# Kernel tuning notes

Measured on AMD Instinct MI355X. Metric: run time of the kernel, lower is better.

The kernel has to match this reference:

```python
import jax, jax.numpy as jnp
import numpy as np

N_SEG = 128      # number of ragged segments (boundaries has N_SEG+1 entries)
SEG_LEN = 128    # tokens per segment (regular boundaries)
D_IN = 1024      # input_size
H = 512          # hidden per direction; output_size = 2*H = 1024


def _run_dir(xs, W_ih, W_hh, b):
    """xs: [L, B, D] -> hidden states [L, B, H] for one direction.
    torch LSTM gate order: i, f, g, o."""
    xp = jnp.einsum('lbd,gd->lbg', xs, W_ih) + b  # precompute input projections [L,B,4H]
    B = xs.shape[1]
    Hh = W_hh.shape[1]

    def step(carry, gx):
        h, c = carry
        g = gx + h @ W_hh.T
        i, f, gg, o = jnp.split(g, 4, axis=-1)
        c = jax.nn.sigmoid(f) * c + jax.nn.sigmoid(i) * jnp.tanh(gg)
        h = jax.nn.sigmoid(o) * jnp.tanh(c)
        return (h, c), h

    z = jnp.zeros((B, Hh), xs.dtype)
    _, hs = jax.lax.scan(step, (z, z), xp)
    return hs


def _bilstm(x, W_ih_f, W_hh_f, b_f, W_ih_b, W_hh_b, b_b):
    hf = _run_dir(x, W_ih_f, W_hh_f, b_f)
    hb = _run_dir(x[::-1], W_ih_b, W_hh_b, b_b)[::-1]
    return jnp.concatenate([hf, hb], axis=-1)  # [L, B, 2H], fwd then bwd as in torch


def setup_inputs() -> dict:
    key = jax.random.key(0)
    ks = jax.random.split(key, 7)
    T = N_SEG * SEG_LEN
    s = 1.0 / np.sqrt(H)  # torch LSTM init scale
    u = lambda k, shape: jax.random.uniform(k, shape, jnp.float32, -s, s)
    return {
        'all_embs': jax.random.normal(ks[0], (T, D_IN), jnp.float32),
        'boundaries': jnp.arange(N_SEG + 1, dtype=jnp.int32) * SEG_LEN,
        'W_ih_f': u(ks[1], (4 * H, D_IN)),
        'W_hh_f': u(ks[2], (4 * H, H)),
        'b_f': u(ks[3], (4 * H,)),  # b_ih + b_hh folded together
        'W_ih_b': u(ks[4], (4 * H, D_IN)),
        'W_hh_b': u(ks[5], (4 * H, H)),
        'b_b': u(ks[6], (4 * H,)),
    }


def reference(all_embs, boundaries, W_ih_f, W_hh_f, b_f, W_ih_b, W_hh_b, b_b):
    n_seg = boundaries.shape[0] - 1
    T, D = all_embs.shape
    L = T // n_seg
    # regular boundaries: batch the per-segment LSTM calls into one scan
    x = all_embs.reshape(n_seg, L, D).transpose(1, 0, 2)  # [L, n_seg, D]
    y = _bilstm(x, W_ih_f, W_hh_f, b_f, W_ih_b, W_hh_b, b_b)  # [L, n_seg, 2H]
    out = y.transpose(1, 0, 2).reshape(T, 2 * H)
    # summarize=False: new boundaries equal old boundaries
    return (out, boundaries)
```

## Files before the change

kernel.cpp:

```cpp
#include <hip/hip_runtime.h>


typedef __attribute__((ext_vector_type(8))) short bf16x8;
typedef __attribute__((ext_vector_type(4))) float f32x4;

__device__ __forceinline__ unsigned short f2bf(float f) {
  unsigned int x = __builtin_bit_cast(unsigned int, f);
  x += 0x7fffu + ((x >> 16) & 1u);
  return (unsigned short)(x >> 16);
}
__device__ __forceinline__ float bf2f(unsigned short u) {
  unsigned int x = ((unsigned int)u) << 16;
  return __builtin_bit_cast(float, x);
}
__device__ __forceinline__ float sigm(float x) { return 1.f / (1.f + __expf(-x)); }
__device__ __forceinline__ float tanhfast(float x) {
  float e = __expf(2.f * x);
  return 1.f - 2.f / (e + 1.f);
}

__device__ __forceinline__ void gl_lds16(const void* g, void* l) {
  __builtin_amdgcn_global_load_lds((const __attribute__((address_space(1))) unsigned int*)g,
                                   (__attribute__((address_space(3))) unsigned int*)l, 16, 0, 0);
}
__device__ __forceinline__ void gl_lds16_llc(const void* g, void* l) {
  __builtin_amdgcn_global_load_lds((const __attribute__((address_space(1))) unsigned int*)g,
                                   (__attribute__((address_space(3))) unsigned int*)l, 16, 0, 17);
}

__global__ __launch_bounds__(256) void cast_x(const float* __restrict__ X,
                                              unsigned short* __restrict__ Xb) {
  const int i = blockIdx.x * 256 + threadIdx.x;
  const float4 v = ((const float4*)X)[i];
  uint2 o;
  o.x = (unsigned int)f2bf(v.x) | ((unsigned int)f2bf(v.y) << 16);
  o.y = (unsigned int)f2bf(v.z) | ((unsigned int)f2bf(v.w) << 16);
  ((uint2*)Xb)[i] = o;
}

__global__ __launch_bounds__(256) void pack_w(const float* __restrict__ Wif,
                                              const float* __restrict__ bf_,
                                              const float* __restrict__ Wib,
                                              const float* __restrict__ bb_,
                                              unsigned short* __restrict__ Wc,
                                              float* __restrict__ biasp) {
  const int pr = blockIdx.x;
  const int d = pr >> 11, r = pr & 2047;
  const float* src = (d ? Wib : Wif) + (size_t)r * 1024;
  const int t = threadIdx.x;
  const float4 v = ((const float4*)src)[t];
  uint2 o;
  o.x = (unsigned int)f2bf(v.x) | ((unsigned int)f2bf(v.y) << 16);
  o.y = (unsigned int)f2bf(v.z) | ((unsigned int)f2bf(v.w) << 16);
  ((uint2*)(Wc + (size_t)pr * 1024))[t] = o;
  if (t == 0) biasp[pr] = (d ? bb_ : bf_)[r];
}

__global__ __launch_bounds__(256) void gemm_xp(const unsigned short* __restrict__ A,
                                               const unsigned short* __restrict__ B,
                                               const float* __restrict__ bias,
                                               unsigned short* __restrict__ C) {
  __shared__ unsigned short As[128 * 64];
  __shared__ unsigned short Bs[128 * 64];
  const int tid = threadIdx.x;
  const int lane = tid & 63;
  const int wid = tid >> 6;
  const int wm = wid >> 1, wn = wid & 1;
  const long brow = (long)blockIdx.x * 128;
  const long bcol = (long)blockIdx.y * 128;

  f32x4 acc[4][4];
  const f32x4 z = {0.f, 0.f, 0.f, 0.f};
#pragma unroll
  for (int i = 0; i < 4; ++i)
#pragma unroll
    for (int j = 0; j < 4; ++j) acc[i][j] = z;

  int srow[4], scol[4];
#pragma unroll
  for (int j = 0; j < 4; ++j) {
    const int o = (j * 256 + tid) * 16;
    srow[j] = o >> 7;
    scol[j] = (o & 127) ^ ((srow[j] & 7) << 4);
  }

  for (int ks = 0; ks < 16; ++ks) {
    const int kb0 = ks * 128;
#pragma unroll
    for (int j = 0; j < 4; ++j) {
      const int o = (j * 256 + tid) * 16;
      gl_lds16((const char*)A + (brow + srow[j]) * 2048 + kb0 + scol[j], (char*)As + o);
      gl_lds16((const char*)B + (bcol + srow[j]) * 2048 + kb0 + scol[j], (char*)Bs + o);
    }
    __syncthreads();
    bf16x8 av[4][2], bv[4][2];
#pragma unroll
    for (int f = 0; f < 4; ++f) {
      const int ra = wm * 64 + f * 16 + (lane & 15);
      const int rb = wn * 64 + f * 16 + (lane & 15);
      const int swa = (ra & 7) << 4, swb = (rb & 7) << 4;
#pragma unroll
      for (int kk = 0; kk < 2; ++kk) {
        const int kby = kk * 64 + (lane >> 4) * 16;
        av[f][kk] = *(const bf16x8*)((const char*)As + ra * 128 + (kby ^ swa));
        bv[f][kk] = *(const bf16x8*)((const char*)Bs + rb * 128 + (kby ^ swb));
      }
    }
#pragma unroll
    for (int kk = 0; kk < 2; ++kk)
#pragma unroll
      for (int fm = 0; fm < 4; ++fm)
#pragma unroll
        for (int fn = 0; fn < 4; ++fn)
          acc[fm][fn] =
              __builtin_amdgcn_mfma_f32_16x16x32_bf16(av[fm][kk], bv[fn][kk], acc[fm][fn], 0, 0, 0);
    __syncthreads();
  }
  const int crow0 = wm * 64 + (lane >> 4) * 4;
  const int ccol0 = wn * 64 + (lane & 15);
#pragma unroll
  for (int fm = 0; fm < 4; ++fm) {
#pragma unroll
    for (int fn = 0; fn < 4; ++fn) {
      const long col = bcol + ccol0 + fn * 16;
      const float bsv = bias[col];
#pragma unroll
      for (int r = 0; r < 4; ++r) {
        const long row = brow + crow0 + fm * 16 + r;
        C[row * 4096 + col] = f2bf(acc[fm][fn][r] + bsv);
      }
    }
  }
}

__global__ __launch_bounds__(256, 1) void lstm_persist(
    const unsigned short* __restrict__ XPb, const float* __restrict__ Whf,
    const float* __restrict__ Whb, unsigned short* __restrict__ hb0,
    unsigned short* __restrict__ hb1, float* __restrict__ out,
    unsigned int* __restrict__ ctr) {
  __shared__ unsigned short A_s[8192];
  __shared__ unsigned short Hrep[16][32];

  const int tid = threadIdx.x;
  const int bid = blockIdx.x;
  const int ut = bid >> 4;
  const int grp = bid & 15;
  const int dir = grp >> 3;
  const int cs = grp & 7;
  const int lane = tid & 63;
  const int w = tid >> 6;
  const int p = lane & 15;
  const int kq8 = lane >> 4;
  const int hi = p >> 3;
  const int u_l = w * 8 + (p & 7);
  const int u_g = ut * 32 + u_l;
  unsigned int* const myctr = ctr + grp * 32;

  bf16x8 wreg[2][16];
  {
    const float* Wh = dir ? Whb : Whf;
#pragma unroll
    for (int f = 0; f < 2; ++f) {
      const int g = f * 2 + hi;
      const float* wrow = Wh + (size_t)(g * 512 + u_g) * 512 + kq8 * 8;
#pragma unroll
      for (int kk = 0; kk < 16; ++kk) {
        const float4 v0 = *(const float4*)(wrow + kk * 32);
        const float4 v1 = *(const float4*)(wrow + kk * 32 + 4);
        bf16x8 t;
        t[0] = (short)f2bf(v0.x); t[1] = (short)f2bf(v0.y);
        t[2] = (short)f2bf(v0.z); t[3] = (short)f2bf(v0.w);
        t[4] = (short)f2bf(v1.x); t[5] = (short)f2bf(v1.y);
        t[6] = (short)f2bf(v1.z); t[7] = (short)f2bf(v1.w);
        wreg[f][kk] = t;
      }
    }
  }

  float c_reg[2] = {0.f, 0.f};
  const size_t tileoff = (size_t)grp * 16384;
  const int cl0 = kq8 * 4 + 2 * hi;

  for (int tau = 0; tau < 128; ++tau) {
    const unsigned short* hc = (tau & 1) ? hb1 : hb0;
    unsigned short* hn = (tau & 1) ? hb0 : hb1;
    const int tcol = dir ? (127 - tau) : tau;

    {
      const char* srcb = (const char*)hc + tileoff;
      char* dstb = (char*)A_s;
#pragma unroll
      for (int j = 0; j < 4; ++j) {
        const int o = (j * 256 + tid) * 16;
        gl_lds16_llc(srcb + o, dstb + o);
      }
    }

    unsigned short xpr[2][4];
#pragma unroll
    for (int j = 0; j < 2; ++j) {
      const int seg = cs * 16 + cl0 + j;
      const size_t tok = (size_t)seg * 128 + tcol;
      const unsigned short* xp = XPb + tok * 4096 + dir * 2048 + u_g;
#pragma unroll
      for (int g = 0; g < 4; ++g) xpr[j][g] = xp[g * 512];
    }
    __syncthreads();

    f32x4 accp[2][2];
    const f32x4 z = {0.f, 0.f, 0.f, 0.f};
    accp[0][0] = z; accp[0][1] = z; accp[1][0] = z; accp[1][1] = z;
    {
      const char* abase = (const char*)A_s + p * 1024;
      const int asw = (p & 7) << 4;
#pragma unroll
      for (int kk = 0; kk < 16; ++kk) {
        const int kb = kk * 64 + kq8 * 16;
        const bf16x8 af = *(const bf16x8*)(abase + (kb ^ asw));
        accp[0][kk & 1] =
            __builtin_amdgcn_mfma_f32_16x16x32_bf16(af, wreg[0][kk], accp[0][kk & 1], 0, 0, 0);
        accp[1][kk & 1] =
            __builtin_amdgcn_mfma_f32_16x16x32_bf16(af, wreg[1][kk], accp[1][kk & 1], 0, 0, 0);
      }
    }
    f32x4 acc0, acc1;
#pragma unroll
    for (int r = 0; r < 4; ++r) {
      acc0[r] = accp[0][0][r] + accp[0][1][r];
      acc1[r] = accp[1][0][r] + accp[1][1][r];
    }

    float hvr[2];
    {
      const float s0 = hi ? acc0[0] : acc0[2];
      const float s1 = hi ? acc0[1] : acc0[3];
      const float s2 = hi ? acc1[0] : acc1[2];
      const float s3 = hi ? acc1[1] : acc1[3];
      const float e0 = __shfl_xor(s0, 8);
      const float e1 = __shfl_xor(s1, 8);
      const float e2 = __shfl_xor(s2, 8);
      const float e3 = __shfl_xor(s3, 8);
      const float a0 = hi ? acc0[2] : acc0[0];
      const float a1 = hi ? acc0[3] : acc0[1];
      const float b0 = hi ? acc1[2] : acc1[0];
      const float b1 = hi ? acc1[3] : acc1[1];
      const float gi[2] = {hi ? e0 : a0, hi ? e1 : a1};
      const float gf[2] = {hi ? a0 : e0, hi ? a1 : e1};
      const float gg[2] = {hi ? e2 : b0, hi ? e3 : b1};
      const float go[2] = {hi ? b0 : e2, hi ? b1 : e3};
#pragma unroll
      for (int j = 0; j < 2; ++j) {
        const int cl = cl0 + j;
        const float pi = gi[j] + bf2f(xpr[j][0]);
        const float pf = gf[j] + bf2f(xpr[j][1]);
        const float pg = gg[j] + bf2f(xpr[j][2]);
        const float po = go[j] + bf2f(xpr[j][3]);
        float cv = sigm(pf) * c_reg[j] + sigm(pi) * tanhfast(pg);
        c_reg[j] = cv;
        hvr[j] = sigm(po) * tanhfast(cv);
        Hrep[cl][u_l] = f2bf(hvr[j]);
      }
    }
    __syncthreads();

    if (tid < 128) {
      const int cl = tid >> 3, q = tid & 7;
      const unsigned long long v = *(const unsigned long long*)&Hrep[cl][q * 4];
      char* dst = (char*)hn + tileoff + cl * 1024 + ((ut * 64 + q * 8) ^ ((cl & 7) << 4));
      __hip_atomic_store((unsigned long long*)dst, v, __ATOMIC_RELAXED,
                         __HIP_MEMORY_SCOPE_AGENT);
    }

    __syncthreads();
    if (tid == 0) {
      const unsigned old =
          __hip_atomic_fetch_add(myctr, 1u, __ATOMIC_RELAXED, __HIP_MEMORY_SCOPE_AGENT);
      const unsigned tgt = (unsigned)(tau + 1) * 16u;
      if (old + 1u != tgt) {
        while (__hip_atomic_load(myctr, __ATOMIC_RELAXED, __HIP_MEMORY_SCOPE_AGENT) < tgt)
          __builtin_amdgcn_s_sleep(1);
      }
    }
#pragma unroll
    for (int j = 0; j < 2; ++j) {
      const int seg = cs * 16 + cl0 + j;
      const size_t tok = (size_t)seg * 128 + tcol;
      out[tok * 1024 + dir * 512 + u_g] = hvr[j];
    }
    __syncthreads();
  }
}

__global__ void wr_bounds(const int* __restrict__ b, float* __restrict__ o) {
  const int i = threadIdx.x;
  if (i < 129) o[i] = (float)b[i];
}

extern "C" void kernel_launch(void* const* d_in, const int* in_sizes, int n_in,
                              void* d_out, int out_size, void* d_ws, size_t ws_size,
                              hipStream_t stream) {
  const float* X = (const float*)d_in[0];
  const int* bnd = (const int*)d_in[1];
  const float* Wif = (const float*)d_in[2];
  const float* Whf = (const float*)d_in[3];
  const float* bf_ = (const float*)d_in[4];
  const float* Wib = (const float*)d_in[5];
  const float* Whb = (const float*)d_in[6];
  const float* bb_ = (const float*)d_in[7];
  float* out = (float*)d_out;

  wr_bounds<<<1, 256, 0, stream>>>(bnd, out + 16777216);

  char* ws = (char*)d_ws;
  const size_t NEED = 176703488ULL;
  if (ws_size < NEED) return;

  unsigned short* XPb = (unsigned short*)(ws + 0);
  unsigned short* Xb = (unsigned short*)(ws + 134217728);
  unsigned short* Wc = (unsigned short*)(ws + 167772160);
  float* biasp = (float*)(ws + 176160768);
  unsigned short* hb0 = (unsigned short*)(ws + 176177152);
  unsigned short* hb1 = (unsigned short*)(ws + 176439296);
  unsigned int* ctrp = (unsigned int*)(ws + 176701440);

  cast_x<<<16384, 256, 0, stream>>>(X, Xb);
  pack_w<<<4096, 256, 0, stream>>>(Wif, bf_, Wib, bb_, Wc, biasp);
  dim3 gg(128, 32);
  gemm_xp<<<gg, 256, 0, stream>>>(Xb, Wc, biasp, XPb);

  hipMemsetAsync(hb0, 0, 262144, stream);
  hipMemsetAsync(ctrp, 0, 2048, stream);

  {
    const unsigned short* xpb = XPb;
    const float* whf = Whf;
    const float* whb = Whb;
    unsigned short* h0 = hb0;
    unsigned short* h1 = hb1;
    float* op = out;
    unsigned int* cp = ctrp;
    void* args[] = {&xpb, &whf, &whb, &h0, &h1, &op, &cp};
    hipError_t e = hipLaunchCooperativeKernel((const void*)lstm_persist, dim3(256), dim3(256),
                                              args, 0, stream);
    if (e != hipSuccess) {
      lstm_persist<<<256, 256, 0, stream>>>(XPb, Whf, Whb, hb0, hb1, out, ctrp);
    }
  }
}
```

Before: 504.9 us.

## Prefetch next-step input projections, defer output stores, stage GEMM epilogue through LDS

The recurrent kernel now loads the next timestep's input-projection values one iteration ahead, so their global-load latency overlaps the current step's MFMA and gate math instead of sitting on the serial path. The output store of h for a step is deferred into the next iteration, after the LDS-load issue, which moves it off the critical path between the barrier spin and the next step. The projection GEMM epilogue writes bf16 results into shared memory and then emits coalesced 16-byte row stores instead of scattered 2-byte stores. In exchange, register pressure rises in the persistent kernel from the extra prefetch and deferred-store registers.

```diff
diff --git a/kernel.cpp b/kernel.cpp
--- a/kernel.cpp
+++ b/kernel.cpp
@@ -60,8 +60,9 @@
                                                const unsigned short* __restrict__ B,
                                                const float* __restrict__ bias,
                                                unsigned short* __restrict__ C) {
-  __shared__ unsigned short As[128 * 64];
-  __shared__ unsigned short Bs[128 * 64];
+  __shared__ unsigned short SMEM[16384];
+  unsigned short* As = SMEM;
+  unsigned short* Bs = SMEM + 8192;
   const int tid = threadIdx.x;
   const int lane = tid & 63;
   const int wid = tid >> 6;
@@ -122,14 +123,20 @@
   for (int fm = 0; fm < 4; ++fm) {
 #pragma unroll
     for (int fn = 0; fn < 4; ++fn) {
-      const long col = bcol + ccol0 + fn * 16;
-      const float bsv = bias[col];
-#pragma unroll
-      for (int r = 0; r < 4; ++r) {
-        const long row = brow + crow0 + fm * 16 + r;
-        C[row * 4096 + col] = f2bf(acc[fm][fn][r] + bsv);
-      }
-    }
+      const int col = ccol0 + fn * 16;
+      const float bsv = bias[bcol + col];
+#pragma unroll
+      for (int r = 0; r < 4; ++r)
+        SMEM[(crow0 + fm * 16 + r) * 128 + col] = f2bf(acc[fm][fn][r] + bsv);
+    }
+  }
+  __syncthreads();
+#pragma unroll
+  for (int j = 0; j < 8; ++j) {
+    const int id = j * 256 + tid;
+    const int row = id >> 4;
+    const int c = id & 15;
+    *(float4*)(C + (brow + row) * 4096 + bcol + c * 8) = *(const float4*)(SMEM + row * 128 + c * 8);
   }
 }
 
@@ -181,6 +188,22 @@
   const size_t tileoff = (size_t)grp * 16384;
   const int cl0 = kq8 * 4 + 2 * hi;
 
+  unsigned short xpr[2][4];
+  {
+    const int tcol0 = dir ? 127 : 0;
+#pragma unroll
+    for (int j = 0; j < 2; ++j) {
+      const int seg = cs * 16 + cl0 + j;
+      const size_t tok = (size_t)seg * 128 + tcol0;
+      const unsigned short* xp = XPb + tok * 4096 + dir * 2048 + u_g;
+#pragma unroll
+      for (int g = 0; g < 4; ++g) xpr[j][g] = xp[g * 512];
+    }
+  }
+
+  float phv[2];
+  size_t pofs[2] = {0, 0};
+
   for (int tau = 0; tau < 128; ++tau) {
     const unsigned short* hc = (tau & 1) ? hb1 : hb0;
     unsigned short* hn = (tau & 1) ? hb0 : hb1;
@@ -195,17 +218,24 @@
         gl_lds16_llc(srcb + o, dstb + o);
       }
     }
-
-    unsigned short xpr[2][4];
-#pragma unroll
-    for (int j = 0; j < 2; ++j) {
-      const int seg = cs * 16 + cl0 + j;
-      const size_t tok = (size_t)seg * 128 + tcol;
-      const unsigned short* xp = XPb + tok * 4096 + dir * 2048 + u_g;
-#pragma unroll
-      for (int g = 0; g < 4; ++g) xpr[j][g] = xp[g * 512];
-    }
-    __syncthreads();
+    if (tau > 0) {
+      out[pofs[0]] = phv[0];
+      out[pofs[1]] = phv[1];
+    }
+    __syncthreads();
+
+    unsigned short xprN[2][4];
+    if (tau < 127) {
+      const int tcolN = dir ? (126 - tau) : (tau + 1);
+#pragma unroll
+      for (int j = 0; j < 2; ++j) {
+        const int seg = cs * 16 + cl0 + j;
+        const size_t tok = (size_t)seg * 128 + tcolN;
+        const unsigned short* xp = XPb + tok * 4096 + dir * 2048 + u_g;
+#pragma unroll
+        for (int g = 0; g < 4; ++g) xprN[j][g] = xp[g * 512];
+      }
+    }
 
     f32x4 accp[2][2];
     const f32x4 z = {0.f, 0.f, 0.f, 0.f};
@@ -259,8 +289,17 @@
         c_reg[j] = cv;
         hvr[j] = sigm(po) * tanhfast(cv);
         Hrep[cl][u_l] = f2bf(hvr[j]);
-      }
-    }
+        const int seg = cs * 16 + cl;
+        const size_t tok = (size_t)seg * 128 + tcol;
+        pofs[j] = tok * 1024 + dir * 512 + u_g;
+        phv[j] = hvr[j];
+      }
+    }
+#pragma unroll
+    for (int j = 0; j < 2; ++j)
+#pragma unroll
+      for (int g = 0; g < 4; ++g) xpr[j][g] = xprN[j][g];
+
     __syncthreads();
 
     if (tid < 128) {
@@ -281,14 +320,10 @@
           __builtin_amdgcn_s_sleep(1);
       }
     }
-#pragma unroll
-    for (int j = 0; j < 2; ++j) {
-      const int seg = cs * 16 + cl0 + j;
-      const size_t tok = (size_t)seg * 128 + tcol;
-      out[tok * 1024 + dir * 512 + u_g] = hvr[j];
-    }
-    __syncthreads();
-  }
+    __syncthreads();
+  }
+  out[pofs[0]] = phv[0];
+  out[pofs[1]] = phv[1];
 }
 
 __global__ void wr_bounds(const int* __restrict__ b, float* __restrict__ o) {
```

New measurement: 502.2 us. Within noise of the previous version (-0.5%).
